# Optimization experiments

Hardware: AMD Instinct MI355X
Metric: run time of the kernel (lower is better)

The kernel has to match this reference:

```python
import jax, jax.numpy as jnp
import numpy as np

N = 120000
G = 64  # voxel grid side
HID = 128
INP = 320
CIN = HID + INP  # 448
K = 27


def _build_neighbor_map(rng):
    # unique occupied voxel cells
    cells = rng.choice(G ** 3, size=N, replace=False)
    xs = cells // (G * G)
    ys = (cells // G) % G
    zs = cells % G
    order = np.argsort(cells)
    sk = cells[order]
    offs = np.array([(dx, dy, dz) for dx in (-1, 0, 1) for dy in (-1, 0, 1) for dz in (-1, 0, 1)], dtype=np.int64)
    nx = xs[:, None] + offs[None, :, 0]
    ny = ys[:, None] + offs[None, :, 1]
    nz = zs[:, None] + offs[None, :, 2]
    valid = (nx >= 0) & (nx < G) & (ny >= 0) & (ny < G) & (nz >= 0) & (nz < G)
    nkey = (nx * G + ny) * G + nz
    pos = np.clip(np.searchsorted(sk, nkey), 0, N - 1)
    found = valid & (sk[pos] == nkey)
    return np.where(found, order[pos], -1).astype(np.int32)  # (N, 27)


def setup_inputs() -> dict:
    key = jax.random.key(0)
    ks = jax.random.split(key, 12)
    rng = np.random.default_rng(0)
    nbr = jnp.asarray(_build_neighbor_map(rng))
    s_conv = 1.0 / np.sqrt(K * CIN)
    s_lin = 1.0 / np.sqrt(CIN)
    return {
        "h": jax.random.normal(ks[0], (N, HID), jnp.float32),
        "x": jax.random.normal(ks[1], (N, INP), jnp.float32),
        "nbr": nbr,
        "Wz": jax.random.normal(ks[2], (K, CIN, HID), jnp.float32) * s_conv,
        "Wz_pt": jax.random.normal(ks[3], (CIN, HID), jnp.float32) * s_lin,
        "bz": jnp.zeros((HID,), jnp.float32),
        "Wr": jax.random.normal(ks[4], (K, CIN, HID), jnp.float32) * s_conv,
        "Wr_pt": jax.random.normal(ks[5], (CIN, HID), jnp.float32) * s_lin,
        "br": jnp.zeros((HID,), jnp.float32),
        "Wq": jax.random.normal(ks[6], (K, CIN, HID), jnp.float32) * s_conv,
        "Wq_pt": jax.random.normal(ks[7], (CIN, HID), jnp.float32) * s_lin,
        "bq": jnp.zeros((HID,), jnp.float32),
    }


def _sconv3d(F, nbr, W, W_pt, b_pt):
    # sparse 3x3x3 conv (gather + matmul accumulate over 27 offsets, no conv bias)
    # followed by voxel_to_point (identity here) + point_transforms linear.
    mask = (nbr >= 0)
    idx = jnp.where(mask, nbr, 0)
    out = F @ W_pt + b_pt  # point transform branch
    for k in range(K):  # fixed small kernel-offset loop
        g = F[idx[:, k]] * mask[:, k:k + 1].astype(F.dtype)  # (N, CIN)
        out = out + g @ W[k]
    return out


def reference(h, x, nbr, Wz, Wz_pt, bz, Wr, Wr_pt, br, Wq, Wq_pt, bq):
    hx = jnp.concatenate([h, x], axis=1)  # (N, 448)
    z = jax.nn.sigmoid(_sconv3d(hx, nbr, Wz, Wz_pt, bz))
    r = jax.nn.sigmoid(_sconv3d(hx, nbr, Wr, Wr_pt, br))
    rx = jnp.concatenate([r * h, x], axis=1)
    q = jnp.tanh(_sconv3d(rx, nbr, Wq, Wq_pt, bq))
    return (1.0 - z) * h + z * q
```

## Files before the change

kernel.cpp:

```cpp
#include <hip/hip_runtime.h>

#define NPTS   120000
#define NOFF   28
#define CHUNKS 7

typedef __bf16 bf16;
typedef __bf16 bf16x8 __attribute__((ext_vector_type(8)));
typedef float  f32x4  __attribute__((ext_vector_type(4)));

__global__ void wprep1(const float* __restrict__ Wz, const float* __restrict__ Wzp,
                       const float* __restrict__ Wr, const float* __restrict__ Wrp,
                       bf16* __restrict__ WB1)
{
    int bid  = blockIdx.x;
    int koff = bid / 56;
    int rem  = bid % 56;
    int ch   = rem / 8;
    int kseg = rem % 8;
    int n    = threadIdx.x;
    int cinb = ch * 64 + kseg * 8;
    bf16x8 v;
    if (n < 128) {
        int col = n;
        #pragma unroll
        for (int j = 0; j < 8; ++j) {
            int cin = cinb + j;
            float w = (koff < 27) ? Wz[((long)koff * 448 + cin) * 128 + col]
                                  : Wzp[(long)cin * 128 + col];
            v[j] = (bf16)w;
        }
    } else {
        int col = n - 128;
        #pragma unroll
        for (int j = 0; j < 8; ++j) {
            int cin = cinb + j;
            float w = (koff < 27) ? Wr[((long)koff * 448 + cin) * 128 + col]
                                  : Wrp[(long)cin * 128 + col];
            v[j] = (bf16)w;
        }
    }
    *(bf16x8*)(WB1 + ((long)bid * 256 + n) * 8) = v;
}

__global__ void wprep2(const float* __restrict__ Wq, const float* __restrict__ Wqp,
                       bf16* __restrict__ WB2)
{
    int bid  = blockIdx.x;
    int koff = bid / 56;
    int rem  = bid % 56;
    int ch   = rem / 8;
    int kseg = rem % 8;
    int n    = threadIdx.x;
    int cinb = ch * 64 + kseg * 8;
    bf16x8 v;
    #pragma unroll
    for (int j = 0; j < 8; ++j) {
        int cin = cinb + j;
        float w = (koff < 27) ? Wq[((long)koff * 448 + cin) * 128 + n]
                              : Wqp[(long)cin * 128 + n];
        v[j] = (bf16)w;
    }
    *(bf16x8*)(WB2 + ((long)bid * 128 + n) * 8) = v;
}

__global__ void fprep(const float* __restrict__ h, const float* __restrict__ x,
                      bf16* __restrict__ F1)
{
    long g = (long)blockIdx.x * blockDim.x + threadIdx.x;
    if (g >= (long)NPTS * 56) return;
    int p = (int)(g / 56);
    int c = (int)(g % 56) * 8;
    const float* src = (c < 128) ? h + (long)p * 128 + c
                                 : x + (long)p * 320 + (c - 128);
    float4 a = ((const float4*)src)[0];
    float4 b = ((const float4*)src)[1];
    bf16x8 v;
    v[0] = (bf16)a.x; v[1] = (bf16)a.y; v[2] = (bf16)a.z; v[3] = (bf16)a.w;
    v[4] = (bf16)b.x; v[5] = (bf16)b.y; v[6] = (bf16)b.z; v[7] = (bf16)b.w;
    *(bf16x8*)(F1 + (long)p * 448 + c) = v;
}

template<int MROWS, int NCOLS, int GATE>
__global__ __launch_bounds__(512)
void gconv(const bf16* __restrict__ F, const int* __restrict__ nbr,
           const bf16* __restrict__ WB, const float* __restrict__ b0,
           const float* __restrict__ b1, const float* __restrict__ hbuf,
           float* __restrict__ zbuf, bf16* __restrict__ f2,
           float* __restrict__ out, const bf16* __restrict__ zrow)
{
    constexpr int THREADS = 512;
    constexpr int MW = MROWS / 64;
    constexpr int AP = 8 * MROWS / THREADS;
    constexpr int BP = 8 * NCOLS / THREADS;

    __shared__ __align__(16) bf16 lA[8 * MROWS * 8];
    __shared__ __align__(16) bf16 lB[8 * NCOLS * 8];
    __shared__ int lidx[MROWS];

    const int t    = threadIdx.x;
    const int lane = t & 63;
    const int w    = t >> 6;
    const int m0   = (w % MW) * 64;
    const int n0   = (w / MW) * 64;
    const int base = blockIdx.x * MROWS;
    const int ar   = t % MROWS;
    const int aks0 = t / MROWS;

    f32x4 acc[4][4];
    #pragma unroll
    for (int i = 0; i < 4; ++i)
        #pragma unroll
        for (int j = 0; j < 4; ++j)
            acc[i][j] = {0.f, 0.f, 0.f, 0.f};

    const bf16x8* lAv = (const bf16x8*)lA;
    const bf16x8* lBv = (const bf16x8*)lB;

    for (int koff = 0; koff < NOFF; ++koff) {
        __syncthreads();
        if (t < MROWS) {
            int p = base + t;
            int idx = -1;
            if (p < NPTS) idx = (koff == 27) ? p : nbr[(long)p * 27 + koff];
            lidx[t] = idx;
        }
        __syncthreads();
        const int myidx = lidx[ar];
        const bf16* row1 = (myidx >= 0) ? (F + (long)myidx * 448) : zrow;
        const bf16* row2 = row1;
        if constexpr (GATE == 2)
            row2 = (myidx >= 0) ? (f2 + (long)myidx * 128) : zrow;

        for (int ch = 0; ch < CHUNKS; ++ch) {
            const bf16* asrc = (GATE == 2 && ch < 2) ? (row2 + ch * 64)
                                                     : (row1 + ch * 64);
            #pragma unroll
            for (int p = 0; p < AP; ++p) {
                int kseg = aks0 + p * (THREADS / MROWS);
                __builtin_amdgcn_global_load_lds(
                    (void*)(asrc + kseg * 8),
                    (void*)(lA + ((long)t + (long)p * THREADS) * 8),
                    16, 0, 0);
            }
            const bf16* bsrc = WB + (long)(koff * CHUNKS + ch) * (NCOLS * 64);
            #pragma unroll
            for (int p = 0; p < BP; ++p) {
                __builtin_amdgcn_global_load_lds(
                    (void*)(bsrc + ((long)t + (long)p * THREADS) * 8),
                    (void*)(lB + ((long)t + (long)p * THREADS) * 8),
                    16, 0, 0);
            }
            __syncthreads();
            #pragma unroll
            for (int kk = 0; kk < 2; ++kk) {
                const int aseg = kk * 4 + (lane >> 4);
                bf16x8 af[4], bfr[4];
                #pragma unroll
                for (int mi = 0; mi < 4; ++mi)
                    af[mi] = lAv[aseg * MROWS + m0 + mi * 16 + (lane & 15)];
                #pragma unroll
                for (int ni = 0; ni < 4; ++ni)
                    bfr[ni] = lBv[aseg * NCOLS + n0 + ni * 16 + (lane & 15)];
                #pragma unroll
                for (int mi = 0; mi < 4; ++mi)
                    #pragma unroll
                    for (int ni = 0; ni < 4; ++ni)
                        acc[mi][ni] = __builtin_amdgcn_mfma_f32_16x16x32_bf16(
                            af[mi], bfr[ni], acc[mi][ni], 0, 0, 0);
            }
            __syncthreads();
        }
    }

    const int quad = lane >> 4;
    const int lc   = lane & 15;
    #pragma unroll
    for (int mi = 0; mi < 4; ++mi) {
        int rb = m0 + mi * 16 + quad * 4;
        #pragma unroll
        for (int ni = 0; ni < 4; ++ni) {
            int c = n0 + ni * 16 + lc;
            f32x4 v = acc[mi][ni];
            #pragma unroll
            for (int rg = 0; rg < 4; ++rg) {
                int p = base + rb + rg;
                if (p < NPTS) {
                    float pre = v[rg];
                    if constexpr (GATE == 1) {
                        if (c < 128) {
                            float z = 1.f / (1.f + __expf(-(pre + b0[c])));
                            zbuf[(long)p * 128 + c] = z;
                        } else {
                            int cc = c - 128;
                            float r = 1.f / (1.f + __expf(-(pre + b1[cc])));
                            f2[(long)p * 128 + cc] = (bf16)(r * hbuf[(long)p * 128 + cc]);
                        }
                    } else {
                        float q  = tanhf(pre + b0[c]);
                        float z  = zbuf[(long)p * 128 + c];
                        float hv = hbuf[(long)p * 128 + c];
                        out[(long)p * 128 + c] = (1.f - z) * hv + z * q;
                    }
                }
            }
        }
    }
}

extern "C" void kernel_launch(void* const* d_in, const int* in_sizes, int n_in,
                              void* d_out, int out_size, void* d_ws, size_t ws_size,
                              hipStream_t stream)
{
    const float* h   = (const float*)d_in[0];
    const float* x   = (const float*)d_in[1];
    const int*   nbr = (const int*)d_in[2];
    const float* Wz  = (const float*)d_in[3];
    const float* Wzp = (const float*)d_in[4];
    const float* bz  = (const float*)d_in[5];
    const float* Wr  = (const float*)d_in[6];
    const float* Wrp = (const float*)d_in[7];
    const float* br  = (const float*)d_in[8];
    const float* Wq  = (const float*)d_in[9];
    const float* Wqp = (const float*)d_in[10];
    const float* bq  = (const float*)d_in[11];
    float* out = (float*)d_out;

    char* ws = (char*)d_ws;
    bf16* WB1 = (bf16*)ws;  ws += (size_t)1568 * 256 * 8 * 2;
    bf16* WB2 = (bf16*)ws;  ws += (size_t)1568 * 128 * 8 * 2;
    bf16* F1  = (bf16*)ws;  ws += (size_t)NPTS * 448 * 2;
    bf16* F2  = (bf16*)ws;  ws += (size_t)NPTS * 128 * 2;
    bf16* zrow = (bf16*)ws; ws += 1024;
    float* zbuf = out;

    hipMemsetAsync(zrow, 0, 1024, stream);
    wprep1<<<1568, 256, 0, stream>>>(Wz, Wzp, Wr, Wrp, WB1);
    wprep2<<<1568, 128, 0, stream>>>(Wq, Wqp, WB2);
    long groups = (long)NPTS * 56;
    fprep<<<(int)((groups + 255) / 256), 256, 0, stream>>>(h, x, F1);

    gconv<128, 256, 1><<<(NPTS + 127) / 128, 512, 0, stream>>>(
        F1, nbr, WB1, bz, br, h, zbuf, F2, nullptr, zrow);
    gconv<256, 128, 2><<<(NPTS + 255) / 256, 512, 0, stream>>>(
        F1, nbr, WB2, bq, nullptr, h, zbuf, F2, out, zrow);
}
```

Baseline: 1.543 ms.

## Replace LDS-staged gather GEMM with register double-buffered direct loads

The gather-conv kernels stop staging A and B tiles through shared memory with barriers. Each wave now loads its gathered feature rows and pre-swizzled weight fragments straight into registers, double-buffered so the next chunk's loads overlap the current MFMAs. The weight prep kernels are rewritten to emit weights already in MFMA fragment order, so B loads coalesce per lane. This removes the LDS traffic and the __syncthreads stalls. In exchange, register pressure rises and weight loads are duplicated across waves that share columns, which leans on the L2 cache.

Result: slower. 2.710 ms (+75.6%).

```diff
diff --git a/kernel.cpp b/kernel.cpp
--- a/kernel.cpp
+++ b/kernel.cpp
@@ -12,55 +12,48 @@
                        const float* __restrict__ Wr, const float* __restrict__ Wrp,
                        bf16* __restrict__ WB1)
 {
-    int bid  = blockIdx.x;
-    int koff = bid / 56;
-    int rem  = bid % 56;
-    int ch   = rem / 8;
-    int kseg = rem % 8;
-    int n    = threadIdx.x;
-    int cinb = ch * 64 + kseg * 8;
+    int tid  = blockIdx.x * 256 + threadIdx.x;
+    int lane = tid & 63;
+    int n16  = (tid >> 6) & 15;
+    int kk   = (tid >> 10) & 1;
+    int chk  = tid >> 11;
+    int koff = chk / 7, ch = chk % 7;
+    int n    = n16 * 16 + (lane & 15);
+    int k0   = ch * 64 + (kk * 4 + (lane >> 4)) * 8;
     bf16x8 v;
-    if (n < 128) {
-        int col = n;
-        #pragma unroll
-        for (int j = 0; j < 8; ++j) {
-            int cin = cinb + j;
-            float w = (koff < 27) ? Wz[((long)koff * 448 + cin) * 128 + col]
-                                  : Wzp[(long)cin * 128 + col];
-            v[j] = (bf16)w;
-        }
-    } else {
-        int col = n - 128;
-        #pragma unroll
-        for (int j = 0; j < 8; ++j) {
-            int cin = cinb + j;
-            float w = (koff < 27) ? Wr[((long)koff * 448 + cin) * 128 + col]
-                                  : Wrp[(long)cin * 128 + col];
-            v[j] = (bf16)w;
-        }
-    }
-    *(bf16x8*)(WB1 + ((long)bid * 256 + n) * 8) = v;
+    #pragma unroll
+    for (int j = 0; j < 8; ++j) {
+        int cin = k0 + j;
+        float w;
+        if (koff < 27) w = (n < 128) ? Wz[((long)koff*448 + cin)*128 + n]
+                                     : Wr[((long)koff*448 + cin)*128 + (n-128)];
+        else           w = (n < 128) ? Wzp[(long)cin*128 + n]
+                                     : Wrp[(long)cin*128 + (n-128)];
+        v[j] = (bf16)w;
+    }
+    *(bf16x8*)(WB1 + (long)tid * 8) = v;
 }
 
 __global__ void wprep2(const float* __restrict__ Wq, const float* __restrict__ Wqp,
                        bf16* __restrict__ WB2)
 {
-    int bid  = blockIdx.x;
-    int koff = bid / 56;
-    int rem  = bid % 56;
-    int ch   = rem / 8;
-    int kseg = rem % 8;
-    int n    = threadIdx.x;
-    int cinb = ch * 64 + kseg * 8;
+    int tid  = blockIdx.x * 256 + threadIdx.x;
+    int lane = tid & 63;
+    int n16  = (tid >> 6) & 7;
+    int kk   = (tid >> 9) & 1;
+    int chk  = tid >> 10;
+    int koff = chk / 7, ch = chk % 7;
+    int n    = n16 * 16 + (lane & 15);
+    int k0   = ch * 64 + (kk * 4 + (lane >> 4)) * 8;
     bf16x8 v;
     #pragma unroll
     for (int j = 0; j < 8; ++j) {
-        int cin = cinb + j;
-        float w = (koff < 27) ? Wq[((long)koff * 448 + cin) * 128 + n]
-                              : Wqp[(long)cin * 128 + n];
+        int cin = k0 + j;
+        float w = (koff < 27) ? Wq[((long)koff*448 + cin)*128 + n]
+                              : Wqp[(long)cin*128 + n];
         v[j] = (bf16)w;
     }
-    *(bf16x8*)(WB2 + ((long)bid * 128 + n) * 8) = v;
+    *(bf16x8*)(WB2 + (long)tid * 8) = v;
 }
 
 __global__ void fprep(const float* __restrict__ h, const float* __restrict__ x,
@@ -70,41 +63,71 @@
     if (g >= (long)NPTS * 56) return;
     int p = (int)(g / 56);
     int c = (int)(g % 56) * 8;
-    const float* src = (c < 128) ? h + (long)p * 128 + c
-                                 : x + (long)p * 320 + (c - 128);
+    const float* src = (c < 128) ? h + (long)p*128 + c : x + (long)p*320 + (c-128);
     float4 a = ((const float4*)src)[0];
     float4 b = ((const float4*)src)[1];
     bf16x8 v;
-    v[0] = (bf16)a.x; v[1] = (bf16)a.y; v[2] = (bf16)a.z; v[3] = (bf16)a.w;
-    v[4] = (bf16)b.x; v[5] = (bf16)b.y; v[6] = (bf16)b.z; v[7] = (bf16)b.w;
-    *(bf16x8*)(F1 + (long)p * 448 + c) = v;
-}
-
-template<int MROWS, int NCOLS, int GATE>
-__global__ __launch_bounds__(512)
-void gconv(const bf16* __restrict__ F, const int* __restrict__ nbr,
-           const bf16* __restrict__ WB, const float* __restrict__ b0,
-           const float* __restrict__ b1, const float* __restrict__ hbuf,
-           float* __restrict__ zbuf, bf16* __restrict__ f2,
-           float* __restrict__ out, const bf16* __restrict__ zrow)
-{
-    constexpr int THREADS = 512;
-    constexpr int MW = MROWS / 64;
-    constexpr int AP = 8 * MROWS / THREADS;
-    constexpr int BP = 8 * NCOLS / THREADS;
-
-    __shared__ __align__(16) bf16 lA[8 * MROWS * 8];
-    __shared__ __align__(16) bf16 lB[8 * NCOLS * 8];
-    __shared__ int lidx[MROWS];
-
+    v[0]=(bf16)a.x; v[1]=(bf16)a.y; v[2]=(bf16)a.z; v[3]=(bf16)a.w;
+    v[4]=(bf16)b.x; v[5]=(bf16)b.y; v[6]=(bf16)b.z; v[7]=(bf16)b.w;
+    *(bf16x8*)(F1 + (long)p*448 + c) = v;
+}
+
+
+#define LOADA(BUF, CH)                                                        \
+    _Pragma("unroll")                                                         \
+    for (int mi = 0; mi < 4; ++mi) {                                          \
+        const bf16* base_;                                                    \
+        if (GATE == 2 && (CH) < 2) base_ = pa2g[mi] + (CH) * 64;              \
+        else                       base_ = pa1[mi] + (CH) * 64;               \
+        af[BUF][mi][0] = *(const bf16x8*)(base_);                             \
+        af[BUF][mi][1] = *(const bf16x8*)(base_ + 32);                        \
+    }
+
+#define LOADB(BUF, KOFF, CH)                                                  \
+    {                                                                         \
+        const bf16x8* p_ = WBv + (((long)((KOFF)*7 + (CH)) * 2) * N16 + wn4) * 64 + lane; \
+        _Pragma("unroll")                                                     \
+        for (int kk = 0; kk < 2; ++kk)                                        \
+            _Pragma("unroll")                                                 \
+            for (int ni = 0; ni < 4; ++ni)                                    \
+                bfr[BUF][ni][kk] = p_[(kk * N16 + ni) * 64];                  \
+    }
+
+#define STEP(CUR, KOFF, CH, IDXN)                                             \
+    {                                                                         \
+        if ((CH) < CHUNKS - 1) { LOADA((CUR)^1, (CH)+1); LOADB((CUR)^1, (KOFF), (CH)+1); } \
+        else if ((KOFF) < NOFF - 1) { setup(IDXN); LOADA((CUR)^1, 0); LOADB((CUR)^1, (KOFF)+1, 0); } \
+        _Pragma("unroll")                                                     \
+        for (int kk = 0; kk < 2; ++kk)                                        \
+            _Pragma("unroll")                                                 \
+            for (int mi = 0; mi < 4; ++mi)                                    \
+                _Pragma("unroll")                                             \
+                for (int ni = 0; ni < 4; ++ni)                                \
+                    acc[mi][ni] = __builtin_amdgcn_mfma_f32_16x16x32_bf16(    \
+                        af[CUR][mi][kk], bfr[CUR][ni][kk], acc[mi][ni], 0, 0, 0); \
+    }
+
+template<int MW, int NW, int GATE>
+__global__ __launch_bounds__(MW * NW * 64, 2)
+void gconv_reg(const bf16* __restrict__ F, const bf16* __restrict__ f2,
+               const int* __restrict__ nbr, const bf16* __restrict__ WB,
+               const float* __restrict__ b0, const float* __restrict__ b1,
+               const float* __restrict__ hbuf, float* __restrict__ zbuf,
+               bf16* __restrict__ f2out, float* __restrict__ out,
+               const bf16* __restrict__ zrow)
+{
+    constexpr int N16 = NW * 64 / 16;
     const int t    = threadIdx.x;
     const int lane = t & 63;
     const int w    = t >> 6;
-    const int m0   = (w % MW) * 64;
-    const int n0   = (w / MW) * 64;
-    const int base = blockIdx.x * MROWS;
-    const int ar   = t % MROWS;
-    const int aks0 = t / MROWS;
+    const int wm   = w % MW;
+    const int wn   = w / MW;
+    const int wn4  = wn * 4;
+    const int mbase = blockIdx.x * (MW * 64) + wm * 64;
+    const int l15  = lane & 15, lq = lane >> 4;
+    const int lrow = mbase + lane;
+
+    const bf16x8* WBv = (const bf16x8*)WB;
 
     f32x4 acc[4][4];
     #pragma unroll
@@ -113,77 +136,48 @@
         for (int j = 0; j < 4; ++j)
             acc[i][j] = {0.f, 0.f, 0.f, 0.f};
 
-    const bf16x8* lAv = (const bf16x8*)lA;
-    const bf16x8* lBv = (const bf16x8*)lB;
-
-    for (int koff = 0; koff < NOFF; ++koff) {
-        __syncthreads();
-        if (t < MROWS) {
-            int p = base + t;
-            int idx = -1;
-            if (p < NPTS) idx = (koff == 27) ? p : nbr[(long)p * 27 + koff];
-            lidx[t] = idx;
+    const bf16* pa1[4];
+    const bf16* pa2g[4];
+
+    auto setup = [&](int idx) {
+        #pragma unroll
+        for (int mi = 0; mi < 4; ++mi) {
+            int r = __shfl(idx, mi * 16 + l15);
+            pa1[mi] = (r >= 0 ? F + (long)r * 448 : zrow) + lq * 8;
+            if constexpr (GATE == 2)
+                pa2g[mi] = (r >= 0 ? f2 + (long)r * 128 : zrow) + lq * 8;
         }
-        __syncthreads();
-        const int myidx = lidx[ar];
-        const bf16* row1 = (myidx >= 0) ? (F + (long)myidx * 448) : zrow;
-        const bf16* row2 = row1;
-        if constexpr (GATE == 2)
-            row2 = (myidx >= 0) ? (f2 + (long)myidx * 128) : zrow;
-
-        for (int ch = 0; ch < CHUNKS; ++ch) {
-            const bf16* asrc = (GATE == 2 && ch < 2) ? (row2 + ch * 64)
-                                                     : (row1 + ch * 64);
-            #pragma unroll
-            for (int p = 0; p < AP; ++p) {
-                int kseg = aks0 + p * (THREADS / MROWS);
-                __builtin_amdgcn_global_load_lds(
-                    (void*)(asrc + kseg * 8),
-                    (void*)(lA + ((long)t + (long)p * THREADS) * 8),
-                    16, 0, 0);
-            }
-            const bf16* bsrc = WB + (long)(koff * CHUNKS + ch) * (NCOLS * 64);
-            #pragma unroll
-            for (int p = 0; p < BP; ++p) {
-                __builtin_amdgcn_global_load_lds(
-                    (void*)(bsrc + ((long)t + (long)p * THREADS) * 8),
-                    (void*)(lB + ((long)t + (long)p * THREADS) * 8),
-                    16, 0, 0);
-            }
-            __syncthreads();
-            #pragma unroll
-            for (int kk = 0; kk < 2; ++kk) {
-                const int aseg = kk * 4 + (lane >> 4);
-                bf16x8 af[4], bfr[4];
-                #pragma unroll
-                for (int mi = 0; mi < 4; ++mi)
-                    af[mi] = lAv[aseg * MROWS + m0 + mi * 16 + (lane & 15)];
-                #pragma unroll
-                for (int ni = 0; ni < 4; ++ni)
-                    bfr[ni] = lBv[aseg * NCOLS + n0 + ni * 16 + (lane & 15)];
-                #pragma unroll
-                for (int mi = 0; mi < 4; ++mi)
-                    #pragma unroll
-                    for (int ni = 0; ni < 4; ++ni)
-                        acc[mi][ni] = __builtin_amdgcn_mfma_f32_16x16x32_bf16(
-                            af[mi], bfr[ni], acc[mi][ni], 0, 0, 0);
-            }
-            __syncthreads();
-        }
-    }
-
-    const int quad = lane >> 4;
-    const int lc   = lane & 15;
+    };
+
+    bf16x8 af[2][4][2], bfr[2][4][2];
+
+    int idx0 = (lrow < NPTS) ? nbr[(long)lrow * 27] : -1;
+    setup(idx0);
+    LOADA(0, 0); LOADB(0, 0, 0);
+
+    for (int kp = 0; kp < NOFF / 2; ++kp) {
+        const int k0 = 2 * kp, k1 = 2 * kp + 1;
+        int idxN0 = -1, idxN1 = -1;
+        if (lrow < NPTS) idxN0 = (k0 + 1 == 27) ? lrow : nbr[(long)lrow * 27 + k0 + 1];
+        STEP(0, k0, 0, idxN0) STEP(1, k0, 1, idxN0) STEP(0, k0, 2, idxN0)
+        STEP(1, k0, 3, idxN0) STEP(0, k0, 4, idxN0) STEP(1, k0, 5, idxN0)
+        STEP(0, k0, 6, idxN0)
+        if (k1 < 27 && lrow < NPTS) idxN1 = nbr[(long)lrow * 27 + k1 + 1];
+        STEP(1, k1, 0, idxN1) STEP(0, k1, 1, idxN1) STEP(1, k1, 2, idxN1)
+        STEP(0, k1, 3, idxN1) STEP(1, k1, 4, idxN1) STEP(0, k1, 5, idxN1)
+        STEP(1, k1, 6, idxN1)
+    }
+
     #pragma unroll
     for (int mi = 0; mi < 4; ++mi) {
-        int rb = m0 + mi * 16 + quad * 4;
+        int rb = mi * 16 + lq * 4;
         #pragma unroll
         for (int ni = 0; ni < 4; ++ni) {
-            int c = n0 + ni * 16 + lc;
+            int c = wn * 64 + ni * 16 + l15;
             f32x4 v = acc[mi][ni];
             #pragma unroll
             for (int rg = 0; rg < 4; ++rg) {
-                int p = base + rb + rg;
+                int p = mbase + rb + rg;
                 if (p < NPTS) {
                     float pre = v[rg];
                     if constexpr (GATE == 1) {
@@ -193,7 +187,7 @@
                         } else {
                             int cc = c - 128;
                             float r = 1.f / (1.f + __expf(-(pre + b1[cc])));
-                            f2[(long)p * 128 + cc] = (bf16)(r * hbuf[(long)p * 128 + cc]);
+                            f2out[(long)p * 128 + cc] = (bf16)(r * hbuf[(long)p * 128 + cc]);
                         }
                     } else {
                         float q  = tanhf(pre + b0[c]);
@@ -226,8 +220,8 @@
     float* out = (float*)d_out;
 
     char* ws = (char*)d_ws;
-    bf16* WB1 = (bf16*)ws;  ws += (size_t)1568 * 256 * 8 * 2;
-    bf16* WB2 = (bf16*)ws;  ws += (size_t)1568 * 128 * 8 * 2;
+    bf16* WB1 = (bf16*)ws;  ws += (size_t)401408 * 8 * 2;
+    bf16* WB2 = (bf16*)ws;  ws += (size_t)200704 * 8 * 2;
     bf16* F1  = (bf16*)ws;  ws += (size_t)NPTS * 448 * 2;
     bf16* F2  = (bf16*)ws;  ws += (size_t)NPTS * 128 * 2;
     bf16* zrow = (bf16*)ws; ws += 1024;
@@ -235,12 +229,12 @@
 
     hipMemsetAsync(zrow, 0, 1024, stream);
     wprep1<<<1568, 256, 0, stream>>>(Wz, Wzp, Wr, Wrp, WB1);
-    wprep2<<<1568, 128, 0, stream>>>(Wq, Wqp, WB2);
+    wprep2<<<784, 256, 0, stream>>>(Wq, Wqp, WB2);
     long groups = (long)NPTS * 56;
     fprep<<<(int)((groups + 255) / 256), 256, 0, stream>>>(h, x, F1);
 
-    gconv<128, 256, 1><<<(NPTS + 127) / 128, 512, 0, stream>>>(
-        F1, nbr, WB1, bz, br, h, zbuf, F2, nullptr, zrow);
-    gconv<256, 128, 2><<<(NPTS + 255) / 256, 512, 0, stream>>>(
-        F1, nbr, WB2, bq, nullptr, h, zbuf, F2, out, zrow);
-}
+    gconv_reg<2, 4, 1><<<(NPTS + 127) / 128, 512, 0, stream>>>(
+        F1, nullptr, nbr, WB1, bz, br, h, zbuf, F2, nullptr, zrow);
+    gconv_reg<4, 2, 2><<<(NPTS + 255) / 256, 512, 0, stream>>>(
+        F1, F2, nbr, WB2, bq, nullptr, h, zbuf, nullptr, out, zrow);
+}
```
